# Optimization experiments

Hardware: AMD Instinct MI355X
Metric: run time of the kernel (lower is better)

## Reference

```python
import jax, jax.numpy as jnp
import numpy as np

B, HK, HV, DK, DV, K = 256, 16, 32, 128, 128, 4
QKV = DK * HK * 2 + DV * HV  # 8192
EPS = 1e-6


def setup_inputs() -> dict:
    key = jax.random.key(0)
    ks = jax.random.split(key, 8)
    return dict(
        mixed_qkv=jax.random.normal(ks[0], (B, QKV), jnp.float32),
        a=jax.random.normal(ks[1], (B, HV), jnp.float32),
        b=jax.random.normal(ks[2], (B, HV), jnp.float32),
        conv_state=jax.random.normal(ks[3], (B, QKV, K - 1), jnp.float32),
        conv_weights=jax.random.normal(ks[4], (QKV, K), jnp.float32) * 0.1,
        dt_bias=jax.random.normal(ks[5], (HV,), jnp.float32),
        alog=jax.random.normal(ks[6], (HV,), jnp.float32) * 0.1,
        ssm_state=jax.random.normal(ks[7], (B, HV, DK, DV), jnp.float32) * 0.05,
    )


def reference(mixed_qkv, a, b, conv_state, conv_weights, dt_bias, alog, ssm_state):
    # --- causal_conv1d_update (decode step, seq=1): window = [cached K-1 steps, new token]
    x_cat = jnp.concatenate([conv_state, mixed_qkv[:, :, None]], axis=-1)  # [B, QKV, K]
    conv_out = jax.nn.silu(jnp.einsum('bck,ck->bc', x_cat, conv_weights))  # [B, QKV]

    # --- split q/k/v heads
    qkv = conv_out.reshape(B, 2 * HK + HV, DK)
    q, k, v = qkv[:, :HK], qkv[:, HK:2 * HK], qkv[:, 2 * HK:]  # [B,HK,DK]x2, [B,HV,DV]

    # --- fused_gdn_gating: g = -exp(A_log) * softplus(a + dt_bias); beta = sigmoid(b)
    g = -jnp.exp(alog)[None, :] * jax.nn.softplus(a + dt_bias[None, :])  # [B, HV]
    beta = jax.nn.sigmoid(b)  # [B, HV]

    # --- GQA expand k heads -> v heads
    rep = HV // HK
    q = jnp.repeat(q, rep, axis=1)  # [B, HV, DK]
    k = jnp.repeat(k, rep, axis=1)

    # --- qk l2-norm (in-kernel) + default scale d_k^-0.5 on q
    q = q / jnp.sqrt(jnp.sum(q * q, axis=-1, keepdims=True) + EPS)
    k = k / jnp.sqrt(jnp.sum(k * k, axis=-1, keepdims=True) + EPS)
    q = q * (DK ** -0.5)

    # --- single-step gated delta rule recurrence
    S = ssm_state * jnp.exp(g)[:, :, None, None]          # decay: [B,HV,DK,DV]
    kv_mem = jnp.einsum('bhkv,bhk->bhv', S, k)            # k^T S
    dv = (v - kv_mem) * beta[:, :, None]                  # delta correction
    S = S + k[:, :, :, None] * dv[:, :, None, :]          # rank-1 update
    o = jnp.einsum('bhkv,bhk->bhv', S, q)                 # [B, HV, DV]
    return o
```

## Files before the change

### kernel.cpp

```cpp
#include <hip/hip_runtime.h>
#include <math.h>

#define NB   256
#define NHK  16
#define NHV  32
#define NDK  128
#define NDV  128
#define NQKV 8192

typedef float f32x4 __attribute__((ext_vector_type(4)));

__global__ __launch_bounds__(256) void gdn_decode_kernel(
    const float* __restrict__ mixed_qkv,
    const float* __restrict__ a_in,
    const float* __restrict__ b_in,
    const float* __restrict__ conv_state,
    const float* __restrict__ conv_w,
    const float* __restrict__ dt_bias,
    const float* __restrict__ alog,
    const float* __restrict__ ssm_state,
    float* __restrict__ out)
{
    const int bid = blockIdx.x;
    const int b   = bid >> 4;
    const int hk  = bid & 15;
    const int tid = threadIdx.x;
    const int h0  = 2 * hk;
    const size_t bh0 = (size_t)b * NHV + h0;

    __shared__ float qL[NDK], kL[NDK], vL[2][NDV];
    __shared__ float redq[128], redk[128], redqk[128];
    __shared__ __align__(16) float p1[8][NDV];
    __shared__ __align__(16) float p2[8][NDV];
    __shared__ float sc_eg[2], sc_beta[2];

    #pragma unroll
    for (int ii = 0; ii < 2; ++ii) {
        int i    = tid + ii * 256;
        int seg  = i >> 7;
        int lane = i & 127;
        int head = (seg == 0) ? hk : (seg == 1) ? (16 + hk) : (32 + h0 + (seg - 2));
        int c    = head * 128 + lane;
        const float* cs = conv_state + ((size_t)b * NQKV + c) * 3;
        const float* w  = conv_w + (size_t)c * 4;
        float x   = mixed_qkv[(size_t)b * NQKV + c];
        float pre = cs[0]*w[0] + cs[1]*w[1] + cs[2]*w[2] + x*w[3];
        float y   = pre / (1.0f + expf(-pre));
        if (seg == 0)      qL[lane] = y;
        else if (seg == 1) kL[lane] = y;
        else               vL[seg - 2][lane] = y;
    }
    if (tid < 2) {
        size_t bh = bh0 + tid;
        int    h  = h0 + tid;
        float av = a_in[bh] + dt_bias[h];
        float sp = fmaxf(av, 0.0f) + log1pf(expf(-fabsf(av)));
        float g  = -expf(alog[h]) * sp;
        sc_eg[tid]   = expf(g);
        sc_beta[tid] = 1.0f / (1.0f + expf(-b_in[bh]));
    }
    __syncthreads();

    if (tid < 128) {
        float qv   = qL[tid];
        redq[tid]  = qv * qv;
        redqk[tid] = qv * kL[tid];
    } else {
        float kv        = kL[tid - 128];
        redk[tid - 128] = kv * kv;
    }
    __syncthreads();
    for (int s = 64; s > 0; s >>= 1) {
        if (tid < s) { redq[tid] += redq[tid + s]; redqk[tid] += redqk[tid + s]; }
        else if (tid >= 128 && tid < 128 + s) { redk[tid-128] += redk[tid-128+s]; }
        __syncthreads();
    }
    const float invq = (1.0f / sqrtf(redq[0] + 1e-6f)) * 0.08838834764831845f;
    const float invk =  1.0f / sqrtf(redk[0] + 1e-6f);
    const float kq   = redqk[0] * invq * invk;
    if (tid < 128) qL[tid] *= invq;
    else           kL[tid - 128] *= invk;
    __syncthreads();

    const int vg = tid & 31;
    const int ks = tid >> 5;
    const f32x4* S0 = (const f32x4*)(ssm_state + bh0 * (NDK * NDV));
    const f32x4* S1 = S0 + (NDK * NDV / 4);
    f32x4 a1_0 = {0.f,0.f,0.f,0.f}, a2_0 = {0.f,0.f,0.f,0.f};
    f32x4 a1_1 = {0.f,0.f,0.f,0.f}, a2_1 = {0.f,0.f,0.f,0.f};
    #pragma unroll
    for (int kk = 0; kk < 16; ++kk) {
        int k = ks * 16 + kk;
        f32x4 s0 = __builtin_nontemporal_load(&S0[k * 32 + vg]);
        f32x4 s1 = __builtin_nontemporal_load(&S1[k * 32 + vg]);
        float kw = kL[k], qw = qL[k];
        a1_0 += s0 * kw;
        a2_0 += s0 * qw;
        a1_1 += s1 * kw;
        a2_1 += s1 * qw;
    }

    *(f32x4*)&p1[ks][vg * 4] = a1_0;
    *(f32x4*)&p2[ks][vg * 4] = a2_0;
    __syncthreads();
    if (tid < 128) {
        float t1 = 0.f, t2 = 0.f;
        #pragma unroll
        for (int s = 0; s < 8; ++s) { t1 += p1[s][tid]; t2 += p2[s][tid]; }
        const float eg   = sc_eg[0];
        const float beta = sc_beta[0];
        float dv = (vL[0][tid] - eg * t1) * beta;
        out[bh0 * NDV + tid] = fmaf(eg, t2, kq * dv);
    }
    __syncthreads();
    *(f32x4*)&p1[ks][vg * 4] = a1_1;
    *(f32x4*)&p2[ks][vg * 4] = a2_1;
    __syncthreads();
    if (tid < 128) {
        float t1 = 0.f, t2 = 0.f;
        #pragma unroll
        for (int s = 0; s < 8; ++s) { t1 += p1[s][tid]; t2 += p2[s][tid]; }
        const float eg   = sc_eg[1];
        const float beta = sc_beta[1];
        float dv = (vL[1][tid] - eg * t1) * beta;
        out[(bh0 + 1) * NDV + tid] = fmaf(eg, t2, kq * dv);
    }
}

extern "C" void kernel_launch(void* const* d_in, const int* in_sizes, int n_in,
                              void* d_out, int out_size, void* d_ws, size_t ws_size,
                              hipStream_t stream) {
    const float* mixed = (const float*)d_in[0];
    const float* a     = (const float*)d_in[1];
    const float* bg    = (const float*)d_in[2];
    const float* cs    = (const float*)d_in[3];
    const float* cw    = (const float*)d_in[4];
    const float* dtb   = (const float*)d_in[5];
    const float* al    = (const float*)d_in[6];
    const float* ssm   = (const float*)d_in[7];
    float* out = (float*)d_out;

    gdn_decode_kernel<<<NB * NHK, 256, 0, stream>>>(mixed, a, bg, cs, cw, dtb, al, ssm, out);
}
```

Before: 97.75 us.

## Prefetch SSM state before conv/norm phase and use wave-shuffle reductions

Issues the first half of each thread's SSM state loads into registers at kernel start, so the memory latency overlaps the convolution, gating and norm computation. The shared-memory tree reduction with its many barriers is replaced by a single-wavefront shuffle reduction of q·q, q·k and k·k. The gating computation moves to threads 64-65 so it does not serialize with the reduction lanes. The prefetch costs 64 extra VGPRs per thread, which may lower occupancy.

```diff
diff --git a/kernel.cpp b/kernel.cpp
--- a/kernel.cpp
+++ b/kernel.cpp
@@ -29,10 +29,23 @@
     const size_t bh0 = (size_t)b * NHV + h0;
 
     __shared__ float qL[NDK], kL[NDK], vL[2][NDV];
-    __shared__ float redq[128], redk[128], redqk[128];
+    __shared__ float red[3];
     __shared__ __align__(16) float p1[8][NDV];
     __shared__ __align__(16) float p2[8][NDV];
     __shared__ float sc_eg[2], sc_beta[2];
+
+    const int vg = tid & 31;
+    const int ks = tid >> 5;
+    const f32x4* S0 = (const f32x4*)(ssm_state + bh0 * (NDK * NDV));
+    const f32x4* S1 = S0 + (NDK * NDV / 4);
+    constexpr int P = 8;
+    f32x4 buf0[P], buf1[P];
+    #pragma unroll
+    for (int kk = 0; kk < P; ++kk) {
+        int k = ks * 16 + kk;
+        buf0[kk] = __builtin_nontemporal_load(&S0[k * 32 + vg]);
+        buf1[kk] = __builtin_nontemporal_load(&S1[k * 32 + vg]);
+    }
 
     #pragma unroll
     for (int ii = 0; ii < 2; ++ii) {
@@ -50,49 +63,47 @@
         else if (seg == 1) kL[lane] = y;
         else               vL[seg - 2][lane] = y;
     }
-    if (tid < 2) {
-        size_t bh = bh0 + tid;
-        int    h  = h0 + tid;
+    if (tid >= 64 && tid < 66) {
+        int    t  = tid - 64;
+        size_t bh = bh0 + t;
+        int    h  = h0 + t;
         float av = a_in[bh] + dt_bias[h];
         float sp = fmaxf(av, 0.0f) + log1pf(expf(-fabsf(av)));
         float g  = -expf(alog[h]) * sp;
-        sc_eg[tid]   = expf(g);
-        sc_beta[tid] = 1.0f / (1.0f + expf(-b_in[bh]));
+        sc_eg[t]   = expf(g);
+        sc_beta[t] = 1.0f / (1.0f + expf(-b_in[bh]));
     }
     __syncthreads();
 
-    if (tid < 128) {
-        float qv   = qL[tid];
-        redq[tid]  = qv * qv;
-        redqk[tid] = qv * kL[tid];
-    } else {
-        float kv        = kL[tid - 128];
-        redk[tid - 128] = kv * kv;
+    if (tid < 64) {
+        float q0 = qL[tid], q1 = qL[tid + 64];
+        float k0 = kL[tid], k1 = kL[tid + 64];
+        float sq  = q0*q0 + q1*q1;
+        float sqk = q0*k0 + q1*k1;
+        float sk  = k0*k0 + k1*k1;
+        #pragma unroll
+        for (int off = 32; off > 0; off >>= 1) {
+            sq  += __shfl_down(sq,  off);
+            sqk += __shfl_down(sqk, off);
+            sk  += __shfl_down(sk,  off);
+        }
+        if (tid == 0) { red[0] = sq; red[1] = sqk; red[2] = sk; }
     }
     __syncthreads();
-    for (int s = 64; s > 0; s >>= 1) {
-        if (tid < s) { redq[tid] += redq[tid + s]; redqk[tid] += redqk[tid + s]; }
-        else if (tid >= 128 && tid < 128 + s) { redk[tid-128] += redk[tid-128+s]; }
-        __syncthreads();
-    }
-    const float invq = (1.0f / sqrtf(redq[0] + 1e-6f)) * 0.08838834764831845f;
-    const float invk =  1.0f / sqrtf(redk[0] + 1e-6f);
-    const float kq   = redqk[0] * invq * invk;
+    const float invq = (1.0f / sqrtf(red[0] + 1e-6f)) * 0.08838834764831845f;
+    const float invk =  1.0f / sqrtf(red[2] + 1e-6f);
+    const float kq   = red[1] * invq * invk;
     if (tid < 128) qL[tid] *= invq;
     else           kL[tid - 128] *= invk;
     __syncthreads();
 
-    const int vg = tid & 31;
-    const int ks = tid >> 5;
-    const f32x4* S0 = (const f32x4*)(ssm_state + bh0 * (NDK * NDV));
-    const f32x4* S1 = S0 + (NDK * NDV / 4);
     f32x4 a1_0 = {0.f,0.f,0.f,0.f}, a2_0 = {0.f,0.f,0.f,0.f};
     f32x4 a1_1 = {0.f,0.f,0.f,0.f}, a2_1 = {0.f,0.f,0.f,0.f};
     #pragma unroll
     for (int kk = 0; kk < 16; ++kk) {
         int k = ks * 16 + kk;
-        f32x4 s0 = __builtin_nontemporal_load(&S0[k * 32 + vg]);
-        f32x4 s1 = __builtin_nontemporal_load(&S1[k * 32 + vg]);
+        f32x4 s0 = (kk < P) ? buf0[kk] : __builtin_nontemporal_load(&S0[k * 32 + vg]);
+        f32x4 s1 = (kk < P) ? buf1[kk] : __builtin_nontemporal_load(&S1[k * 32 + vg]);
         float kw = kL[k], qw = qL[k];
         a1_0 += s0 * kw;
         a2_0 += s0 * qw;
```

Result: faster. 88.73 us (-9.2%).
